# Performance work log

Measured on AMD Instinct MI355X. Metric: run time of the kernel, lower is better.

## Reference

```python
import jax, jax.numpy as jnp
import numpy as np

G = 7          # grid_size
A = 2          # anchors_per_cell
C = 3          # num_classes
L_COORD, L_OBJ, L_NOOBJ, L_CLS = 5.0, 1.0, 0.5, 2.0


def setup_inputs() -> dict:
    key = jax.random.key(0)
    k0, k1, k2, k3, k4 = jax.random.split(key, 5)
    B, M = 32768, 20
    predictions = jax.random.normal(k0, (B, G, G, A, 5 + C), dtype=jnp.float32)
    xy1 = jax.random.uniform(k1, (B, M, 2), dtype=jnp.float32) * 0.8
    wh = jax.random.uniform(k2, (B, M, 2), dtype=jnp.float32) * 0.19 + 0.01
    target_boxes = jnp.concatenate([xy1, xy1 + wh], axis=-1)  # valid x1<x2, y1<y2
    target_labels = jax.random.randint(k3, (B, M), 0, C, dtype=jnp.int32)
    num_objs = jax.random.randint(k4, (B,), 0, M + 1, dtype=jnp.int32)
    anchors = jnp.array([[0.971, 1.7338], [3.4579, 5.1653]], dtype=jnp.float32)
    class_weights = jnp.array([1.0, 4.9, 4.8], dtype=jnp.float32)
    return dict(predictions=predictions, target_boxes=target_boxes,
                target_labels=target_labels, num_objs=num_objs,
                anchors=anchors, class_weights=class_weights)


def assign_targets(target_boxes, target_labels, num_objs, anchors, B):
    """Vectorized scatter-based replacement of the nested python assignment loop."""
    M = target_boxes.shape[1]
    x1, y1, x2, y2 = [target_boxes[..., i] for i in range(4)]  # (B,M)
    cx, cy = (x1 + x2) * 0.5, (y1 + y2) * 0.5
    w, h = x2 - x1, y2 - y1
    valid = (w > 0) & (h > 0) & (jnp.arange(M)[None, :] < num_objs[:, None])
    gi = jnp.clip(jnp.floor(cy * G).astype(jnp.int32), 0, G - 1)
    gj = jnp.clip(jnp.floor(cx * G).astype(jnp.int32), 0, G - 1)
    wg, hg = w * G, h * G
    # anchor matching IoU (width/height only), (B,M,A)
    inter = jnp.minimum(wg[..., None], anchors[:, 0]) * jnp.minimum(hg[..., None], anchors[:, 1])
    union = (wg * hg)[..., None] + anchors[:, 0] * anchors[:, 1] - inter
    best_a = jnp.argmax(inter / (union + 1e-6), axis=-1).astype(jnp.int32)  # first max = torch loop tie-break
    aw = anchors[best_a, 0]
    ah = anchors[best_a, 1]
    tx = cx * G - gj.astype(jnp.float32)
    ty = cy * G - gi.astype(jnp.float32)
    tw = jnp.log(jnp.clip(wg, 0.01, None) / (aw + 1e-6))
    th = jnp.log(jnp.clip(hg, 0.01, None) / (ah + 1e-6))
    tvals = jnp.stack([tx, ty, tw, th], axis=-1)  # (B,M,4)
    N = B * G * G * A
    bidx = jnp.arange(B, dtype=jnp.int32)[:, None]
    flat = ((bidx * G + gi) * G + gj) * A + best_a  # (B,M)
    flat = jnp.where(valid, flat, N)                # invalid -> dropped by scatter
    idx = flat.ravel()
    obj_mask = jnp.zeros((N,), jnp.float32).at[idx].set(1.0, mode='drop')
    target_bbox = jnp.zeros((N, 4), jnp.float32).at[idx].set(tvals.reshape(-1, 4), mode='drop')
    target_cls = jnp.zeros((N,), jnp.int32).at[idx].set(target_labels.ravel(), mode='drop')
    shape = (B, G, G, A)
    return obj_mask.reshape(shape), target_bbox.reshape(shape + (4,)), target_cls.reshape(shape)


def reference(predictions, target_boxes, target_labels, num_objs, anchors, class_weights):
    B = predictions.shape[0]
    pred_obj = predictions[..., 0]
    pred_bbox = predictions[..., 1:5]
    pred_cls = predictions[..., 5:]
    m, target_bbox, target_cls = assign_targets(target_boxes, target_labels, num_objs, anchors, B)
    sp = jax.nn.softplus
    # BCE-with-logits: target is 1 on obj cells, 0 on noobj cells
    loss_obj = jnp.sum(m * sp(-pred_obj))
    loss_noobj = jnp.sum((1.0 - m) * sp(pred_obj))
    # smooth L1 (beta=1), summed over obj cells
    d = pred_bbox - target_bbox
    ad = jnp.abs(d)
    sl1 = jnp.where(ad < 1.0, 0.5 * d * d, ad - 0.5)
    loss_bbox = jnp.sum(m[..., None] * sl1)
    # weighted cross entropy on obj cells
    logZ = jax.nn.logsumexpimport if False else jax.scipy.special.logsumexp(pred_cls, axis=-1)
    logit_t = jnp.take_along_axis(pred_cls, target_cls[..., None], axis=-1)[..., 0]
    loss_cls = jnp.sum(m * class_weights[target_cls] * (logZ - logit_t))
    num_pos = jnp.maximum(jnp.sum(m), 1.0)
    total = (L_COORD * loss_bbox + L_OBJ * loss_obj + L_NOOBJ * loss_noobj + L_CLS * loss_cls) / num_pos
    return total
```

## Files before the change

kernel.cpp:

```cpp
#include <hip/hip_runtime.h>


namespace {
constexpr int kG = 7;
constexpr int kA = 2;
constexpr int kM = 20;
constexpr int kCells = kG * kG * kA;
constexpr int kCh = 8;
constexpr int kNB = 32;
constexpr int kBlock = 448;
constexpr int kTgt = kNB * kM;
constexpr int kChunks = kNB * kCells * 2;
constexpr int kIters = kChunks / kBlock;
}

__device__ __forceinline__ float softplus_fast(float x) {
    return fmaxf(x, 0.0f) + __logf(1.0f + __expf(-fabsf(x)));
}

__global__ __launch_bounds__(kBlock) void det_loss_main(
    const float* __restrict__ preds,
    const float* __restrict__ tboxes,
    const int* __restrict__ tlabels,
    const int* __restrict__ nobjs,
    const float* __restrict__ anchors,
    const float* __restrict__ cweights,
    float* __restrict__ partial,
    int B)
{
    __shared__ float4 s_tv[kTgt];
    __shared__ short  s_cell[kTgt];
    __shared__ int    s_pos[kTgt];
    __shared__ int    s_nobj[kNB];
    __shared__ int    s_npos;
    __shared__ float  s_red[kBlock / 64][4];

    const int tid = threadIdx.x;
    const int b0 = blockIdx.x * kNB;

    if (tid < kNB) {
        const int b = b0 + tid;
        s_nobj[tid] = (b < B) ? nobjs[b] : 0;
    }
    if (tid == 0) s_npos = 0;
    __syncthreads();

    const float a00 = anchors[0], a01 = anchors[1];
    const float a10 = anchors[2], a11 = anchors[3];

    for (int j = tid; j < kTgt; j += kBlock) {
        const int bl = j / kM;
        const int m  = j - bl * kM;
        short cell = -1;
        float4 tv = make_float4(0.f, 0.f, 0.f, 0.f);
        if (b0 + bl < B) {
            const float4 box = ((const float4*)tboxes)[(size_t)b0 * kM + j];
            const float x1 = box.x, y1 = box.y, x2 = box.z, y2 = box.w;
            const float cx = (x1 + x2) * 0.5f, cy = (y1 + y2) * 0.5f;
            const float w = x2 - x1, h = y2 - y1;
            if (w > 0.f && h > 0.f && m < s_nobj[bl]) {
                const int gi = min(max((int)floorf(cy * (float)kG), 0), kG - 1);
                const int gj = min(max((int)floorf(cx * (float)kG), 0), kG - 1);
                const float wg = w * (float)kG, hg = h * (float)kG;
                const float i0 = fminf(wg, a00) * fminf(hg, a01);
                const float u0 = wg * hg + a00 * a01 - i0;
                const float r0 = i0 / (u0 + 1e-6f);
                const float i1 = fminf(wg, a10) * fminf(hg, a11);
                const float u1 = wg * hg + a10 * a11 - i1;
                const float r1 = i1 / (u1 + 1e-6f);
                const int a = (r1 > r0) ? 1 : 0;
                const float aw = a ? a10 : a00;
                const float ah = a ? a11 : a01;
                tv.x = cx * (float)kG - (float)gj;
                tv.y = cy * (float)kG - (float)gi;
                tv.z = __logf(fmaxf(wg, 0.01f) / (aw + 1e-6f));
                tv.w = __logf(fmaxf(hg, 0.01f) / (ah + 1e-6f));
                cell = (short)(bl * kCells + (gi * kG + gj) * kA + a);
            }
        }
        s_cell[j] = cell;
        s_tv[j] = tv;
    }
    __syncthreads();

    for (int j = tid; j < kTgt; j += kBlock) {
        const short c = s_cell[j];
        if (c >= 0) {
            const int bl = j / kM;
            const int m  = j - bl * kM;
            bool win = true;
            for (int m2 = m + 1; m2 < kM; ++m2) {
                if (s_cell[bl * kM + m2] == c) { win = false; break; }
            }
            if (win) {
                const int idx = atomicAdd(&s_npos, 1);
                s_pos[idx] = (j << 16) | (int)c;
            }
        }
    }
    __syncthreads();

    float accO = 0.f, accN = 0.f, accB = 0.f, accC = 0.f;
    const float* __restrict__ pblk = preds + (size_t)b0 * kCells * kCh;
    const float4* __restrict__ pblk4 = (const float4*)pblk;
    if (b0 + kNB <= B) {
        const bool hasObj = (tid & 1) == 0;
        #pragma unroll
        for (int k = 0; k < kIters; ++k) {
            const float4 v = pblk4[(size_t)(tid + k * kBlock)];
            if (hasObj) accN += softplus_fast(v.x);
        }
    } else {
        const int nchunk = (B - b0) * kCells * 2;
        const bool hasObj = (tid & 1) == 0;
        for (int i = tid; i < nchunk; i += kBlock) {
            const float4 v = pblk4[(size_t)i];
            if (hasObj) accN += softplus_fast(v.x);
        }
    }

    const int np = s_npos;
    const float cw0 = cweights[0], cw1 = cweights[1], cw2 = cweights[2];
    for (int t = tid; t < np; t += kBlock) {
        const int pk = s_pos[t];
        const int j  = pk >> 16;
        const int ci = pk & 0xFFFF;
        const float4* pc = (const float4*)(pblk + (size_t)ci * kCh);
        const float4 p0 = pc[0];
        const float4 p1 = pc[1];
        const float spp = softplus_fast(p0.x);
        accN -= spp;
        accO += spp - p0.x;
        const float4 tv = s_tv[j];
        float d, ad;
        d = p0.y - tv.x; ad = fabsf(d); accB += (ad < 1.f) ? 0.5f * d * d : ad - 0.5f;
        d = p0.z - tv.y; ad = fabsf(d); accB += (ad < 1.f) ? 0.5f * d * d : ad - 0.5f;
        d = p0.w - tv.z; ad = fabsf(d); accB += (ad < 1.f) ? 0.5f * d * d : ad - 0.5f;
        d = p1.x - tv.w; ad = fabsf(d); accB += (ad < 1.f) ? 0.5f * d * d : ad - 0.5f;
        const int lab = tlabels[(size_t)b0 * kM + j];
        const float c0 = p1.y, c1 = p1.z, c2 = p1.w;
        const float mx = fmaxf(c0, fmaxf(c1, c2));
        const float lse = mx + __logf(__expf(c0 - mx) + __expf(c1 - mx) + __expf(c2 - mx));
        const float logit = (lab == 0) ? c0 : ((lab == 1) ? c1 : c2);
        const float cwv   = (lab == 0) ? cw0 : ((lab == 1) ? cw1 : cw2);
        accC += cwv * (lse - logit);
    }

    float vals[4] = {accO, accN, accB, accC};
    #pragma unroll
    for (int k = 0; k < 4; ++k) {
        float v = vals[k];
        #pragma unroll
        for (int off = 32; off > 0; off >>= 1) v += __shfl_down(v, off, 64);
        vals[k] = v;
    }
    const int wave = tid >> 6;
    const int lane = tid & 63;
    if (lane == 0) {
        #pragma unroll
        for (int k = 0; k < 4; ++k) s_red[wave][k] = vals[k];
    }
    __syncthreads();
    if (tid == 0) {
        const int nb = gridDim.x;
        #pragma unroll
        for (int k = 0; k < 4; ++k) {
            float t = 0.f;
            #pragma unroll
            for (int w = 0; w < kBlock / 64; ++w) t += s_red[w][k];
            partial[(size_t)k * nb + blockIdx.x] = t;
        }
        partial[(size_t)4 * nb + blockIdx.x] = (float)np;
    }
}

__global__ __launch_bounds__(256) void det_loss_reduce(
    const float* __restrict__ partial, int nblocks, float* __restrict__ out)
{
    __shared__ float s_red[4][5];
    const int tid = threadIdx.x;
    float v[5] = {0.f, 0.f, 0.f, 0.f, 0.f};
    for (int i = tid; i < nblocks; i += 256) {
        #pragma unroll
        for (int k = 0; k < 5; ++k) v[k] += partial[(size_t)k * nblocks + i];
    }
    #pragma unroll
    for (int k = 0; k < 5; ++k) {
        float x = v[k];
        #pragma unroll
        for (int off = 32; off > 0; off >>= 1) x += __shfl_down(x, off, 64);
        v[k] = x;
    }
    const int wave = tid >> 6;
    const int lane = tid & 63;
    if (lane == 0) {
        #pragma unroll
        for (int k = 0; k < 5; ++k) s_red[wave][k] = v[k];
    }
    __syncthreads();
    if (tid == 0) {
        float t[5];
        #pragma unroll
        for (int k = 0; k < 5; ++k) {
            float s = 0.f;
            #pragma unroll
            for (int w = 0; w < 4; ++w) s += s_red[w][k];
            t[k] = s;
        }
        const float npv = fmaxf(t[4], 1.0f);
        out[0] = (5.0f * t[2] + 1.0f * t[0] + 0.5f * t[1] + 2.0f * t[3]) / npv;
    }
}

extern "C" void kernel_launch(void* const* d_in, const int* in_sizes, int n_in,
                              void* d_out, int out_size, void* d_ws, size_t ws_size,
                              hipStream_t stream) {
    const float* preds    = (const float*)d_in[0];
    const float* tboxes   = (const float*)d_in[1];
    const int*   tlabels  = (const int*)d_in[2];
    const int*   nobjs    = (const int*)d_in[3];
    const float* anchors  = (const float*)d_in[4];
    const float* cweights = (const float*)d_in[5];
    float* out = (float*)d_out;
    float* partial = (float*)d_ws;

    const int B = in_sizes[0] / (kCells * kCh);
    const int blocks = (B + kNB - 1) / kNB;

    det_loss_main<<<blocks, kBlock, 0, stream>>>(
        preds, tboxes, tlabels, nobjs, anchors, cweights, partial, B);
    det_loss_reduce<<<1, 256, 0, stream>>>(partial, blocks, out);
}
```

Measured before the change: 184.2 us.

## Split noobj softplus streaming into separate grid-stride kernel

```diff
diff --git a/kernel.cpp b/kernel.cpp
--- a/kernel.cpp
+++ b/kernel.cpp
@@ -8,17 +8,17 @@
 constexpr int kCells = kG * kG * kA;
 constexpr int kCh = 8;
 constexpr int kNB = 32;
-constexpr int kBlock = 448;
+constexpr int kBlockA = 448;
 constexpr int kTgt = kNB * kM;
-constexpr int kChunks = kNB * kCells * 2;
-constexpr int kIters = kChunks / kBlock;
+constexpr int kBlockN = 256;
+constexpr int kGridN = 2048;
 }
 
 __device__ __forceinline__ float softplus_fast(float x) {
     return fmaxf(x, 0.0f) + __logf(1.0f + __expf(-fabsf(x)));
 }
 
-__global__ __launch_bounds__(kBlock) void det_loss_main(
+__global__ __launch_bounds__(kBlockA) void det_loss_assign(
     const float* __restrict__ preds,
     const float* __restrict__ tboxes,
     const int* __restrict__ tlabels,
@@ -26,14 +26,14 @@
     const float* __restrict__ anchors,
     const float* __restrict__ cweights,
     float* __restrict__ partial,
-    int B)
+    int B, int NT)
 {
     __shared__ float4 s_tv[kTgt];
     __shared__ short  s_cell[kTgt];
     __shared__ int    s_pos[kTgt];
     __shared__ int    s_nobj[kNB];
     __shared__ int    s_npos;
-    __shared__ float  s_red[kBlock / 64][4];
+    __shared__ float  s_red[kBlockA / 64][4];
 
     const int tid = threadIdx.x;
     const int b0 = blockIdx.x * kNB;
@@ -48,7 +48,7 @@
     const float a00 = anchors[0], a01 = anchors[1];
     const float a10 = anchors[2], a11 = anchors[3];
 
-    for (int j = tid; j < kTgt; j += kBlock) {
+    for (int j = tid; j < kTgt; j += kBlockA) {
         const int bl = j / kM;
         const int m  = j - bl * kM;
         short cell = -1;
@@ -83,7 +83,7 @@
     }
     __syncthreads();
 
-    for (int j = tid; j < kTgt; j += kBlock) {
+    for (int j = tid; j < kTgt; j += kBlockA) {
         const short c = s_cell[j];
         if (c >= 0) {
             const int bl = j / kM;
@@ -102,26 +102,9 @@
 
     float accO = 0.f, accN = 0.f, accB = 0.f, accC = 0.f;
     const float* __restrict__ pblk = preds + (size_t)b0 * kCells * kCh;
-    const float4* __restrict__ pblk4 = (const float4*)pblk;
-    if (b0 + kNB <= B) {
-        const bool hasObj = (tid & 1) == 0;
-        #pragma unroll
-        for (int k = 0; k < kIters; ++k) {
-            const float4 v = pblk4[(size_t)(tid + k * kBlock)];
-            if (hasObj) accN += softplus_fast(v.x);
-        }
-    } else {
-        const int nchunk = (B - b0) * kCells * 2;
-        const bool hasObj = (tid & 1) == 0;
-        for (int i = tid; i < nchunk; i += kBlock) {
-            const float4 v = pblk4[(size_t)i];
-            if (hasObj) accN += softplus_fast(v.x);
-        }
-    }
-
     const int np = s_npos;
     const float cw0 = cweights[0], cw1 = cweights[1], cw2 = cweights[2];
-    for (int t = tid; t < np; t += kBlock) {
+    for (int t = tid; t < np; t += kBlockA) {
         const int pk = s_pos[t];
         const int j  = pk >> 16;
         const int ci = pk & 0xFFFF;
@@ -162,27 +145,72 @@
     }
     __syncthreads();
     if (tid == 0) {
-        const int nb = gridDim.x;
         #pragma unroll
         for (int k = 0; k < 4; ++k) {
             float t = 0.f;
             #pragma unroll
-            for (int w = 0; w < kBlock / 64; ++w) t += s_red[w][k];
-            partial[(size_t)k * nb + blockIdx.x] = t;
-        }
-        partial[(size_t)4 * nb + blockIdx.x] = (float)np;
+            for (int w = 0; w < kBlockA / 64; ++w) t += s_red[w][k];
+            partial[(size_t)k * NT + blockIdx.x] = t;
+        }
+        partial[(size_t)4 * NT + blockIdx.x] = (float)np;
+    }
+}
+
+__global__ __launch_bounds__(kBlockN) void det_loss_noobj(
+    const float4* __restrict__ preds4,
+    float* __restrict__ partial,
+    long long n4, int NT, int col0)
+{
+    __shared__ float s_red[kBlockN / 64];
+    const int tid = threadIdx.x;
+    const long long gtid = (long long)blockIdx.x * kBlockN + tid;
+    const long long stride = (long long)gridDim.x * kBlockN;
+    const bool hasObj = ((gtid & 1) == 0);
+    float acc = 0.f;
+    long long i = gtid;
+    for (; i + 3 * stride < n4; i += 4 * stride) {
+        const float4 v0 = preds4[i];
+        const float4 v1 = preds4[i + stride];
+        const float4 v2 = preds4[i + 2 * stride];
+        const float4 v3 = preds4[i + 3 * stride];
+        if (hasObj) {
+            acc += softplus_fast(v0.x);
+            acc += softplus_fast(v1.x);
+            acc += softplus_fast(v2.x);
+            acc += softplus_fast(v3.x);
+        }
+    }
+    for (; i < n4; i += stride) {
+        const float4 v = preds4[i];
+        if (hasObj) acc += softplus_fast(v.x);
+    }
+
+    #pragma unroll
+    for (int off = 32; off > 0; off >>= 1) acc += __shfl_down(acc, off, 64);
+    if ((tid & 63) == 0) s_red[tid >> 6] = acc;
+    __syncthreads();
+    if (tid == 0) {
+        float t = 0.f;
+        #pragma unroll
+        for (int w = 0; w < kBlockN / 64; ++w) t += s_red[w];
+        const int col = col0 + blockIdx.x;
+        partial[(size_t)0 * NT + col] = 0.f;
+        partial[(size_t)1 * NT + col] = t;
+        partial[(size_t)2 * NT + col] = 0.f;
+        partial[(size_t)3 * NT + col] = 0.f;
+        partial[(size_t)4 * NT + col] = 0.f;
     }
 }
 
 __global__ __launch_bounds__(256) void det_loss_reduce(
-    const float* __restrict__ partial, int nblocks, float* __restrict__ out)
+    const float* __restrict__ partial, int NT, float* __restrict__ out)
 {
     __shared__ float s_red[4][5];
     const int tid = threadIdx.x;
     float v[5] = {0.f, 0.f, 0.f, 0.f, 0.f};
-    for (int i = tid; i < nblocks; i += 256) {
-        #pragma unroll
-        for (int k = 0; k < 5; ++k) v[k] += partial[(size_t)k * nblocks + i];
+    for (int i = tid; i < NT; i += 256) {
+        #pragma unroll
+        for (int k = 0; k < 5; ++k) v[k] += partial[(size_t)k * NT + i];
     }
     #pragma unroll
     for (int k = 0; k < 5; ++k) {
@@ -225,9 +253,13 @@
     float* partial = (float*)d_ws;
 
     const int B = in_sizes[0] / (kCells * kCh);
-    const int blocks = (B + kNB - 1) / kNB;
-
-    det_loss_main<<<blocks, kBlock, 0, stream>>>(
-        preds, tboxes, tlabels, nobjs, anchors, cweights, partial, B);
-    det_loss_reduce<<<1, 256, 0, stream>>>(partial, blocks, out);
-}
+    const int blocksA = (B + kNB - 1) / kNB;
+    const int NT = blocksA + kGridN;
+    const long long n4 = (long long)B * kCells * 2;
+
+    det_loss_assign<<<blocksA, kBlockA, 0, stream>>>(
+        preds, tboxes, tlabels, nobjs, anchors, cweights, partial, B, NT);
+    det_loss_noobj<<<kGridN, kBlockN, 0, stream>>>(
+        (const float4*)preds, partial, n4, NT, blocksA);
+    det_loss_reduce<<<1, 256, 0, stream>>>(partial, NT, out);
+}
```

Measured after the change: 186.9 us. About the same (+1.5%).
